# Optimization experiments

Hardware: AMD Instinct MI355X
Metric: run time of the kernel (lower is better)

Reference implementation:

```python
import jax, jax.numpy as jnp
import numpy as np
import math

EMBED_DIM = 1024
NUM_HEADS = 16
HEAD_DIM = EMBED_DIM // NUM_HEADS
B, S = 2, 2048


def setup_inputs() -> dict:
    key = jax.random.key(0)
    ks = jax.random.split(key, 5)
    scale = 1.0 / math.sqrt(EMBED_DIM)
    x = jax.random.normal(ks[0], (B, S, EMBED_DIM), dtype=jnp.float32)
    W_q = jax.random.normal(ks[1], (EMBED_DIM, EMBED_DIM), dtype=jnp.float32) * scale
    W_k = jax.random.normal(ks[2], (EMBED_DIM, EMBED_DIM), dtype=jnp.float32) * scale
    W_v = jax.random.normal(ks[3], (EMBED_DIM, EMBED_DIM), dtype=jnp.float32) * scale
    W_o = jax.random.normal(ks[4], (EMBED_DIM, EMBED_DIM), dtype=jnp.float32) * scale
    # causal mask: True = masked out (matches torch masked_fill semantics)
    mask = jnp.triu(jnp.ones((S, S), dtype=bool), k=1)
    return {"x": x, "mask": mask, "W_q": W_q, "W_k": W_k, "W_v": W_v, "W_o": W_o}


def _split_heads(x):
    b, s, _ = x.shape
    return x.reshape(b, s, NUM_HEADS, HEAD_DIM).transpose(0, 2, 1, 3)  # [b,h,s,hd]


def reference(x, mask, W_q, W_k, W_v, W_o):
    # torch nn.Linear(bias=False): y = x @ W.T
    Q = _split_heads(x @ W_q.T)
    K = _split_heads(x @ W_k.T)
    V = _split_heads(x @ W_v.T)
    scale = 1.0 / math.sqrt(HEAD_DIM)
    scores = jnp.einsum("bhqd,bhkd->bhqk", Q, K) * scale  # [b,h,s,s]
    scores = jnp.where(mask[None, None, :, :], -jnp.inf, scores)
    weights = jax.nn.softmax(scores, axis=-1)
    out = jnp.einsum("bhqk,bhkd->bhqd", weights, V)
    out = out.transpose(0, 2, 1, 3).reshape(x.shape[0], x.shape[1], EMBED_DIM)
    return out @ W_o.T
```

## Files before the change

kernel.cpp:

```cpp
#include <hip/hip_runtime.h>
#include <hip/hip_bf16.h>

typedef short bf16x8 __attribute__((ext_vector_type(8)));
typedef unsigned short u16x8 __attribute__((ext_vector_type(8)));
typedef unsigned short u16x4 __attribute__((ext_vector_type(4)));
typedef float f32x4 __attribute__((ext_vector_type(4)));

typedef unsigned int __attribute__((address_space(1))) gu32;
typedef unsigned int __attribute__((address_space(3))) lu32;

#define MFMA16(a, b, c) __builtin_amdgcn_mfma_f32_16x16x32_bf16((a), (b), (c), 0, 0, 0)

constexpr int SEQ = 2048;
constexpr int NH = 16;
constexpr int NTOK = 2 * SEQ;

__device__ __forceinline__ float bf2f(unsigned short u) {
  union { unsigned int i; float f; } v; v.i = ((unsigned int)u) << 16; return v.f;
}
__device__ __forceinline__ unsigned short f2bf(float f) {
  __hip_bfloat16 h = __float2bfloat16(f);
  return __builtin_bit_cast(unsigned short, h);
}
__device__ __forceinline__ unsigned int pkbf_trunc(float hi, float lo) {
  return __builtin_amdgcn_perm(__builtin_bit_cast(unsigned int, hi),
                               __builtin_bit_cast(unsigned int, lo), 0x07060302u);
}
__device__ __forceinline__ u16x8 cvt8(const float* __restrict__ p) {
  f32x4 a = *(const f32x4*)p;
  f32x4 b = *(const f32x4*)(p + 4);
  u16x8 r;
#pragma unroll
  for (int j = 0; j < 4; j++) { r[j] = f2bf(a[j]); r[4 + j] = f2bf(b[j]); }
  return r;
}

__global__ __launch_bounds__(256) void cvt_all(
    const float* __restrict__ x, const float* __restrict__ wq, const float* __restrict__ wk,
    const float* __restrict__ wv, const float* __restrict__ wo,
    unsigned short* __restrict__ Xb, unsigned short* __restrict__ Wb) {
  const int z = blockIdx.y;
  const float* src = (z == 0) ? x : (z == 1) ? wq : (z == 2) ? wk : (z == 3) ? wv : wo;
  unsigned short* dst = (z == 0) ? Xb : Wb + (size_t)(z - 1) * 1024 * 1024;
  const int n = (z == 0) ? NTOK * 1024 : 1024 * 1024;
  for (int i = (blockIdx.x * 256 + threadIdx.x) * 8; i < n; i += gridDim.x * 256 * 8)
    *(u16x8*)(dst + i) = cvt8(src + i);
}

template <int ROWS, int NWAVE>
__device__ __forceinline__ void stage_glds(const unsigned short* __restrict__ gbase,
                                           int rstride,
                                           unsigned short* __restrict__ lds,
                                           int wid, int lane) {
  constexpr int ISS = ROWS * 8 / (NWAVE * 64);
#pragma unroll
  for (int t = 0; t < ISS; ++t) {
    const int slot = (wid * ISS + t) * 64 + lane;
    const int row = slot >> 3;
    const int c8 = (slot & 7) ^ (row & 7);
    const unsigned short* gp = gbase + (size_t)row * rstride + c8 * 8;
    unsigned short* lp = lds + (size_t)(wid * ISS + t) * 512;
    __builtin_amdgcn_global_load_lds((const gu32*)gp, (lu32*)lp, 16, 0, 0);
  }
}

__device__ __forceinline__ bf16x8 frag_ld(const unsigned short* __restrict__ lds, int row, int c8) {
  const int slot = row * 8 + (c8 ^ (row & 7));
  return *(const bf16x8*)(lds + slot * 8);
}

template <int BM, int BN, int LDC, bool CF32>
__global__ __launch_bounds__(256) void gemm_lds(
    const unsigned short* __restrict__ A,
    const unsigned short* __restrict__ B,
    void* __restrict__ Cv) {
  constexpr int K = 1024;
  constexpr int MI = BM / 32, NI = BN / 32;

  __shared__ __align__(16) unsigned short As[BM * 64];
  __shared__ __align__(16) unsigned short Bs[BN * 64];

  const int tid = threadIdx.x;
  const int wid = tid >> 6;
  const int lane = tid & 63;
  const int quad = lane >> 4;
  const int c16 = lane & 15;
  const int wrow = wid >> 1, wcol = wid & 1;

  const int m0 = blockIdx.x * BM;
  const int n0 = blockIdx.y * BN;

  f32x4 acc[MI][NI];
#pragma unroll
  for (int i = 0; i < MI; i++)
#pragma unroll
    for (int j = 0; j < NI; j++) acc[i][j] = f32x4{0.f, 0.f, 0.f, 0.f};

  for (int kb = 0; kb < K; kb += 64) {
    __syncthreads();
    stage_glds<BM, 4>(A + (size_t)m0 * K + kb, K, As, wid, lane);
    stage_glds<BN, 4>(B + (size_t)n0 * K + kb, K, Bs, wid, lane);
    __syncthreads();
#pragma unroll
    for (int ks = 0; ks < 2; ++ks) {
      bf16x8 af[MI], bfr[NI];
#pragma unroll
      for (int i = 0; i < MI; i++)
        af[i] = frag_ld(As, wrow * (BM / 2) + i * 16 + c16, ks * 4 + quad);
#pragma unroll
      for (int j = 0; j < NI; j++)
        bfr[j] = frag_ld(Bs, wcol * (BN / 2) + j * 16 + c16, ks * 4 + quad);
#pragma unroll
      for (int i = 0; i < MI; i++)
#pragma unroll
        for (int j = 0; j < NI; j++) acc[i][j] = MFMA16(af[i], bfr[j], acc[i][j]);
    }
  }

#pragma unroll
  for (int i = 0; i < MI; i++) {
#pragma unroll
    for (int j = 0; j < NI; j++) {
      int row = m0 + wrow * (BM / 2) + i * 16 + quad * 4;
      int col = n0 + wcol * (BN / 2) + j * 16 + c16;
#pragma unroll
      for (int r = 0; r < 4; r++) {
        if constexpr (CF32) ((float*)Cv)[(size_t)(row + r) * LDC + col] = acc[i][j][r];
        else ((unsigned short*)Cv)[(size_t)(row + r) * LDC + col] = f2bf(acc[i][j][r]);
      }
    }
  }
}

__device__ __forceinline__ int vt_idx(int d, int kv) {
  int ck = kv >> 3;
  int s = ((d >> 3) ^ d) & 7;
  return d * 64 + ((ck ^ s) << 3) + (kv & 7);
}

struct AttnShared {
  unsigned short Kt[2][64 * 64];
  unsigned short Vt[64 * 64];
  unsigned short Pt[4][16 * 72];
};

__global__ __launch_bounds__(256) void attn_kernel(
    const unsigned short* __restrict__ QKV,
    unsigned short* __restrict__ Oa) {
  __shared__ AttnShared sh;
  const int h = blockIdx.x;
  const int b = blockIdx.y;
  const int t = 31 - blockIdx.z;
  const int tid = threadIdx.x;
  const int wid = tid >> 6, lane = tid & 63;
  const int quad = lane >> 4, c16 = lane & 15;
  const size_t tokbase = (size_t)b * SEQ;
  const int q0 = t * 64;
  const int nkv = t + 1;

  const unsigned short* qp = QKV + (tokbase + q0 + wid * 16 + c16) * 3072 + h * 64;
  bf16x8 qf[2];
#pragma unroll
  for (int ks = 0; ks < 2; ++ks) {
    u16x8 u = *(const u16x8*)(qp + ks * 32 + quad * 8);
    bf16x8 tq;
#pragma unroll
    for (int j = 0; j < 8; j++) tq[j] = (short)f2bf(0.1803368801f * bf2f(u[j]));
    qf[ks] = tq;
  }

  const unsigned short* kbase = QKV + tokbase * 3072 + 1024 + h * 64;
  const unsigned short* vbase = QKV + tokbase * 3072 + 2048 + h * 64;
  const int vkv = (tid >> 4) * 4;
  const int vd = (tid & 15) * 4;

  f32x4 o[4];
  float lacc = 0.f;
#pragma unroll
  for (int nt = 0; nt < 4; nt++) o[nt] = f32x4{0.f, 0.f, 0.f, 0.f};
  unsigned short* PtW = sh.Pt[wid];

  stage_glds<64, 4>(kbase, 3072, sh.Kt[0], wid, lane);
  u16x4 vr[4];
#pragma unroll
  for (int i = 0; i < 4; i++)
    vr[i] = *(const u16x4*)(vbase + (size_t)(vkv + i) * 3072 + vd);

  for (int kt = 0; kt < nkv; ++kt) {
    const int buf = kt & 1;
    __syncthreads();
#pragma unroll
    for (int dd = 0; dd < 4; ++dd) {
      uint2 w;
      w.x = (unsigned int)vr[0][dd] | ((unsigned int)vr[1][dd] << 16);
      w.y = (unsigned int)vr[2][dd] | ((unsigned int)vr[3][dd] << 16);
      *(uint2*)&sh.Vt[vt_idx(vd + dd, vkv)] = w;
    }
    __syncthreads();

    if (kt + 1 < nkv) {
      const size_t nofs = (size_t)(kt + 1) * 64;
      stage_glds<64, 4>(kbase + nofs * 3072, 3072, sh.Kt[buf ^ 1], wid, lane);
#pragma unroll
      for (int i = 0; i < 4; i++)
        vr[i] = *(const u16x4*)(vbase + (nofs + vkv + i) * 3072 + vd);
    }

    const unsigned short* KtB = sh.Kt[buf];
    f32x4 st[4];
#pragma unroll
    for (int nt = 0; nt < 4; ++nt) {
      f32x4 a = f32x4{-16.f, -16.f, -16.f, -16.f};
      a = MFMA16(frag_ld(KtB, nt * 16 + c16, quad), qf[0], a);
      a = MFMA16(frag_ld(KtB, nt * 16 + c16, 4 + quad), qf[1], a);
      st[nt] = a;
    }
    if (kt == nkv - 1) {
      const int kv0 = kt * 64;
      const int qg = q0 + wid * 16 + c16;
#pragma unroll
      for (int nt = 0; nt < 4; nt++)
#pragma unroll
        for (int r = 0; r < 4; r++) {
          int kg = kv0 + nt * 16 + quad * 4 + r;
          if (kg > qg) st[nt][r] = -1e30f;
        }
    }

#pragma unroll
    for (int nt = 0; nt < 4; nt++) {
      float p0 = __builtin_amdgcn_exp2f(st[nt][0]);
      float p1 = __builtin_amdgcn_exp2f(st[nt][1]);
      float p2 = __builtin_amdgcn_exp2f(st[nt][2]);
      float p3 = __builtin_amdgcn_exp2f(st[nt][3]);
      lacc += (p0 + p1) + (p2 + p3);
      uint2 w;
      w.x = pkbf_trunc(p1, p0);
      w.y = pkbf_trunc(p3, p2);
      *(uint2*)&PtW[c16 * 72 + nt * 16 + quad * 4] = w;
    }

#pragma unroll
    for (int ks = 0; ks < 2; ++ks) {
      bf16x8 pf = *(const bf16x8*)&PtW[c16 * 72 + ks * 32 + quad * 8];
#pragma unroll
      for (int nt2 = 0; nt2 < 4; ++nt2) {
        bf16x8 vf = *(const bf16x8*)&sh.Vt[vt_idx(nt2 * 16 + c16, ks * 32 + quad * 8)];
        o[nt2] = MFMA16(vf, pf, o[nt2]);
      }
    }
  }

  lacc += __shfl_xor(lacc, 16);
  lacc += __shfl_xor(lacc, 32);
  const float linv = 1.f / lacc;
  const size_t row = tokbase + q0 + wid * 16 + c16;
#pragma unroll
  for (int nt2 = 0; nt2 < 4; nt2++) {
    uint2 w;
    w.x = (unsigned int)f2bf(o[nt2][0] * linv) | ((unsigned int)f2bf(o[nt2][1] * linv) << 16);
    w.y = (unsigned int)f2bf(o[nt2][2] * linv) | ((unsigned int)f2bf(o[nt2][3] * linv) << 16);
    *(uint2*)&Oa[row * 1024 + h * 64 + nt2 * 16 + quad * 4] = w;
  }
}

template <int BM, int BN, int LDC, bool AF32, bool CF32>
__global__ __launch_bounds__(256) void gemm_bt(
    const void* __restrict__ Av, const float* __restrict__ W0, const float* __restrict__ W1,
    const float* __restrict__ W2, void* __restrict__ Cv) {
  constexpr int K = 1024;
  constexpr int LDS_LD = 72;
  constexpr int MI = BM / 32, NI = BN / 32;
  __shared__ __align__(16) unsigned short As[BM][LDS_LD];
  __shared__ __align__(16) unsigned short Bs[BN][LDS_LD];
  const int tid = threadIdx.x, wid = tid >> 6, lane = tid & 63;
  const int quad = lane >> 4, c16 = lane & 15;
  const int wrow = wid >> 1, wcol = wid & 1;
  const float* W = (blockIdx.z == 0) ? W0 : (blockIdx.z == 1 ? W1 : W2);
  const int m0 = blockIdx.y * BM, n0 = blockIdx.x * BN, cofs = blockIdx.z * 1024;
  f32x4 acc[MI][NI];
#pragma unroll
  for (int i = 0; i < MI; i++)
#pragma unroll
    for (int j = 0; j < NI; j++) acc[i][j] = f32x4{0.f, 0.f, 0.f, 0.f};
  for (int kb = 0; kb < K; kb += 64) {
    __syncthreads();
#pragma unroll
    for (int c = tid; c < BM * 8; c += 256) {
      int row = c >> 3, c8 = c & 7;
      if constexpr (AF32)
        *(u16x8*)&As[row][c8 * 8] = cvt8((const float*)Av + (size_t)(m0 + row) * K + kb + c8 * 8);
      else
        *(u16x8*)&As[row][c8 * 8] = *(const u16x8*)((const unsigned short*)Av + (size_t)(m0 + row) * K + kb + c8 * 8);
    }
#pragma unroll
    for (int c = tid; c < BN * 8; c += 256) {
      int row = c >> 3, c8 = c & 7;
      *(u16x8*)&Bs[row][c8 * 8] = cvt8(W + (size_t)(n0 + row) * K + kb + c8 * 8);
    }
    __syncthreads();
#pragma unroll
    for (int ks = 0; ks < 2; ++ks) {
      bf16x8 af[MI], bfr[NI];
#pragma unroll
      for (int i = 0; i < MI; i++)
        af[i] = *(const bf16x8*)&As[wrow * (BM / 2) + i * 16 + c16][ks * 32 + quad * 8];
#pragma unroll
      for (int j = 0; j < NI; j++)
        bfr[j] = *(const bf16x8*)&Bs[wcol * (BN / 2) + j * 16 + c16][ks * 32 + quad * 8];
#pragma unroll
      for (int i = 0; i < MI; i++)
#pragma unroll
        for (int j = 0; j < NI; j++) acc[i][j] = MFMA16(af[i], bfr[j], acc[i][j]);
    }
  }
#pragma unroll
  for (int i = 0; i < MI; i++)
#pragma unroll
    for (int j = 0; j < NI; j++) {
      int row = m0 + wrow * (BM / 2) + i * 16 + quad * 4;
      int col = n0 + wcol * (BN / 2) + j * 16 + c16 + cofs;
#pragma unroll
      for (int r = 0; r < 4; r++) {
        if constexpr (CF32) ((float*)Cv)[(size_t)(row + r) * LDC + col] = acc[i][j][r];
        else ((unsigned short*)Cv)[(size_t)(row + r) * LDC + col] = f2bf(acc[i][j][r]);
      }
    }
}

extern "C" void kernel_launch(void* const* d_in, const int* in_sizes, int n_in,
                              void* d_out, int out_size, void* d_ws, size_t ws_size,
                              hipStream_t stream) {
  const float* x = (const float*)d_in[0];
  const float* Wq = (const float*)d_in[2];
  const float* Wk = (const float*)d_in[3];
  const float* Wv = (const float*)d_in[4];
  const float* Wo = (const float*)d_in[5];
  float* out = (float*)d_out;

  unsigned short* QKV = (unsigned short*)d_ws;
  unsigned short* Wb = QKV + (size_t)NTOK * 3072;
  unsigned short* Xb = Wb + (size_t)4 * 1024 * 1024;
  unsigned short* AT = Xb;

  if (ws_size >= (size_t)40 * 1024 * 1024) {
    cvt_all<<<dim3(256, 5), 256, 0, stream>>>(x, Wq, Wk, Wv, Wo, Xb, Wb);
    gemm_lds<128, 64, 3072, false><<<dim3(32, 48), 256, 0, stream>>>(Xb, Wb, QKV);
    attn_kernel<<<dim3(NH, 2, 32), 256, 0, stream>>>(QKV, AT);
    gemm_lds<128, 64, 1024, true><<<dim3(32, 16), 256, 0, stream>>>(
        AT, Wb + (size_t)3 * 1024 * 1024, out);
  } else {
    unsigned short* QKV2 = (unsigned short*)d_ws;
    unsigned short* AT2 = QKV2 + (size_t)NTOK * 3072;
    gemm_bt<128, 128, 3072, true, false><<<dim3(8, 32, 3), 256, 0, stream>>>(x, Wq, Wk, Wv, QKV2);
    attn_kernel<<<dim3(NH, 2, 32), 256, 0, stream>>>(QKV2, AT2);
    gemm_bt<64, 64, 1024, false, true><<<dim3(16, 64, 1), 256, 0, stream>>>(AT2, Wo, Wo, Wo, out);
  }
}
```

Measured before the change: 182.8 us.

## Replace QKV projection GEMM with 256x256-tile eight-phase pipelined kernel

Adds a new QKV projection GEMM that uses 256x256 output tiles with 512 threads and double-buffered LDS filled by direct global-to-LDS loads. The loop is split into eight phases, interleaving fragment loads, async stage issues, and prioritized MFMA blocks between explicit barriers, with an XCD-aware block swizzle over 192 blocks. The aim is higher data reuse per tile and overlap of memory traffic with matrix math in the largest GEMM. The cost is 128 KB of LDS per block, many barriers, and only 192 blocks, which is below one wave of blocks per CU.

```diff
diff --git a/kernel.cpp b/kernel.cpp
--- a/kernel.cpp
+++ b/kernel.cpp
@@ -128,6 +128,140 @@
         if constexpr (CF32) ((float*)Cv)[(size_t)(row + r) * LDC + col] = acc[i][j][r];
         else ((unsigned short*)Cv)[(size_t)(row + r) * LDC + col] = f2bf(acc[i][j][r]);
       }
+    }
+  }
+}
+
+#define SBAR do { __builtin_amdgcn_sched_barrier(0); \
+                  asm volatile("s_barrier" ::: "memory"); \
+                  __builtin_amdgcn_sched_barrier(0); } while (0)
+
+__global__ __launch_bounds__(512) void gemm_8ph(
+    const unsigned short* __restrict__ A,
+    const unsigned short* __restrict__ B,
+    unsigned short* __restrict__ C) {
+  constexpr int K = 1024;
+  __shared__ __align__(16) unsigned short As[2][256 * 64];
+  __shared__ __align__(16) unsigned short Bs[2][256 * 64];
+
+  const int tid = threadIdx.x;
+  const int wid = tid >> 6, lane = tid & 63;
+  const int quad = lane >> 4, c16 = lane & 15;
+  const int wr = wid >> 2;
+  const int wc = wid & 3;
+
+  const int bid = blockIdx.x;
+  const int swz = (bid & 7) * 24 + (bid >> 3);
+  const int m0 = (swz / 12) * 256;
+  const int n0 = (swz % 12) * 256;
+
+  const unsigned short* Abase = A + (size_t)m0 * K;
+  const unsigned short* Bbase = B + (size_t)n0 * K;
+
+  f32x4 acc[8][4];
+#pragma unroll
+  for (int i = 0; i < 8; i++)
+#pragma unroll
+    for (int j = 0; j < 4; j++) acc[i][j] = f32x4{0.f, 0.f, 0.f, 0.f};
+
+  bf16x8 af[4][2];
+  bf16x8 bf0[2][2];
+  bf16x8 bf1[2][2];
+
+  auto lda = [&](const unsigned short* asb, int mo) {
+#pragma unroll
+    for (int mi = 0; mi < 4; mi++)
+#pragma unroll
+      for (int ks = 0; ks < 2; ks++)
+        af[mi][ks] = frag_ld(asb, wr * 128 + mo + mi * 16 + c16, ks * 4 + quad);
+  };
+  auto ldb = [&](const unsigned short* bsb, bf16x8 (&bf)[2][2], int no) {
+#pragma unroll
+    for (int ni = 0; ni < 2; ni++)
+#pragma unroll
+      for (int ks = 0; ks < 2; ks++)
+        bf[ni][ks] = frag_ld(bsb, wc * 64 + no + ni * 16 + c16, ks * 4 + quad);
+  };
+  auto mmq = [&](bf16x8 (&bf)[2][2], int mo, int no) {
+    __builtin_amdgcn_s_setprio(1);
+#pragma unroll
+    for (int mi = 0; mi < 4; mi++)
+#pragma unroll
+      for (int ni = 0; ni < 2; ni++)
+#pragma unroll
+        for (int ks = 0; ks < 2; ks++)
+          acc[mo + mi][no + ni] = MFMA16(af[mi][ks], bf[ni][ks], acc[mo + mi][no + ni]);
+    __builtin_amdgcn_s_setprio(0);
+  };
+
+  stage_glds<128, 8>(Bbase, K, Bs[0], wid, lane);
+  stage_glds<128, 8>(Bbase + (size_t)128 * K, K, Bs[0] + 8192, wid, lane);
+  stage_glds<128, 8>(Abase, K, As[0], wid, lane);
+  stage_glds<128, 8>(Abase + (size_t)128 * K, K, As[0] + 8192, wid, lane);
+  stage_glds<128, 8>(Bbase + 64, K, Bs[1], wid, lane);
+  stage_glds<128, 8>(Bbase + (size_t)128 * K + 64, K, Bs[1] + 8192, wid, lane);
+  asm volatile("s_waitcnt vmcnt(4)" ::: "memory");
+  SBAR;
+
+  for (int i = 0; i < 7; ++i) {
+    const int t = 2 * i;
+    const int kb1 = (t + 1) * 64, kb2 = (t + 2) * 64, kb3 = (t + 3) * 64;
+    lda(As[0], 0); ldb(Bs[0], bf0, 0);
+    stage_glds<128, 8>(Abase + kb1, K, As[1], wid, lane);
+    SBAR; mmq(bf0, 0, 0); SBAR;
+    ldb(Bs[0], bf1, 32);
+    stage_glds<128, 8>(Abase + (size_t)128 * K + kb1, K, As[1] + 8192, wid, lane);
+    SBAR; mmq(bf1, 0, 2); SBAR;
+    lda(As[0], 64);
+    stage_glds<128, 8>(Bbase + kb2, K, Bs[0], wid, lane);
+    SBAR; mmq(bf0, 4, 0); SBAR;
+    stage_glds<128, 8>(Bbase + (size_t)128 * K + kb2, K, Bs[0] + 8192, wid, lane);
+    asm volatile("s_waitcnt vmcnt(4)" ::: "memory");
+    SBAR; mmq(bf1, 4, 2); SBAR;
+    lda(As[1], 0); ldb(Bs[1], bf0, 0);
+    stage_glds<128, 8>(Abase + kb2, K, As[0], wid, lane);
+    SBAR; mmq(bf0, 0, 0); SBAR;
+    ldb(Bs[1], bf1, 32);
+    stage_glds<128, 8>(Abase + (size_t)128 * K + kb2, K, As[0] + 8192, wid, lane);
+    SBAR; mmq(bf1, 0, 2); SBAR;
+    lda(As[1], 64);
+    stage_glds<128, 8>(Bbase + kb3, K, Bs[1], wid, lane);
+    SBAR; mmq(bf0, 4, 0); SBAR;
+    stage_glds<128, 8>(Bbase + (size_t)128 * K + kb3, K, Bs[1] + 8192, wid, lane);
+    asm volatile("s_waitcnt vmcnt(4)" ::: "memory");
+    SBAR; mmq(bf1, 4, 2); SBAR;
+  }
+
+  {
+    const int kb1 = 15 * 64;
+    lda(As[0], 0); ldb(Bs[0], bf0, 0);
+    stage_glds<128, 8>(Abase + kb1, K, As[1], wid, lane);
+    SBAR; mmq(bf0, 0, 0); SBAR;
+    ldb(Bs[0], bf1, 32);
+    stage_glds<128, 8>(Abase + (size_t)128 * K + kb1, K, As[1] + 8192, wid, lane);
+    SBAR; mmq(bf1, 0, 2); SBAR;
+    lda(As[0], 64);
+    SBAR; mmq(bf0, 4, 0); SBAR;
+    asm volatile("s_waitcnt vmcnt(0)" ::: "memory");
+    SBAR; mmq(bf1, 4, 2); SBAR;
+    lda(As[1], 0); ldb(Bs[1], bf0, 0);
+    SBAR; mmq(bf0, 0, 0); SBAR;
+    ldb(Bs[1], bf1, 32);
+    SBAR; mmq(bf1, 0, 2); SBAR;
+    lda(As[1], 64);
+    SBAR; mmq(bf0, 4, 0); SBAR;
+    SBAR; mmq(bf1, 4, 2);
+  }
+
+#pragma unroll
+  for (int mi = 0; mi < 8; mi++) {
+#pragma unroll
+    for (int ni = 0; ni < 4; ni++) {
+      const int row = m0 + wr * 128 + mi * 16 + quad * 4;
+      const int col = n0 + wc * 64 + ni * 16 + c16;
+#pragma unroll
+      for (int r = 0; r < 4; r++)
+        C[(size_t)(row + r) * 3072 + col] = f2bf(acc[mi][ni][r]);
     }
   }
 }
@@ -345,7 +479,7 @@
 
   if (ws_size >= (size_t)40 * 1024 * 1024) {
     cvt_all<<<dim3(256, 5), 256, 0, stream>>>(x, Wq, Wk, Wv, Wo, Xb, Wb);
-    gemm_lds<128, 64, 3072, false><<<dim3(32, 48), 256, 0, stream>>>(Xb, Wb, QKV);
+    gemm_8ph<<<dim3(192), 512, 0, stream>>>(Xb, Wb, QKV);
     attn_kernel<<<dim3(NH, 2, 32), 256, 0, stream>>>(QKV, AT);
     gemm_lds<128, 64, 1024, true><<<dim3(32, 16), 256, 0, stream>>>(
         AT, Wb + (size_t)3 * 1024 * 1024, out);
```

Result: faster. 178.8 us (-2.2%).

## Replace QKV projection GEMM with 256x192 eight-phase pipelined kernel

Applied to the files above, without the earlier changes.

Adds a new 512-thread QKV GEMM with 256x192 output tiles, double-buffered LDS, async global-to-LDS staging interleaved with MFMA phases under explicit barriers and vmcnt waits, and a swizzled block order. It targets the latency and low reuse of the previous 128x64 tile GEMM. It also raises wave priority around the MFMA sections in the attention kernel. The hand-scheduled phases depend on exact vmcnt accounting and use a large LDS footprint, which limits occupancy.

```diff
diff --git a/kernel.cpp b/kernel.cpp
--- a/kernel.cpp
+++ b/kernel.cpp
@@ -128,6 +128,134 @@
         if constexpr (CF32) ((float*)Cv)[(size_t)(row + r) * LDC + col] = acc[i][j][r];
         else ((unsigned short*)Cv)[(size_t)(row + r) * LDC + col] = f2bf(acc[i][j][r]);
       }
+    }
+  }
+}
+
+#define SBAR do { __builtin_amdgcn_sched_barrier(0); \
+                  asm volatile("s_barrier" ::: "memory"); \
+                  __builtin_amdgcn_sched_barrier(0); } while (0)
+
+__global__ __launch_bounds__(512) void gemm_8ph_w192(
+    const unsigned short* __restrict__ A,
+    const unsigned short* __restrict__ B,
+    unsigned short* __restrict__ C) {
+  constexpr int K = 1024;
+  __shared__ __align__(16) unsigned short As[2][256 * 64];
+  __shared__ __align__(16) unsigned short Bs[2][192 * 64];
+
+  const int tid = threadIdx.x;
+  const int wid = tid >> 6, lane = tid & 63;
+  const int quad = lane >> 4, c16 = lane & 15;
+  const int wr = wid >> 2;
+  const int wc = wid & 3;
+
+  const int bid = blockIdx.x;
+  const int swz = (bid & 7) * 32 + (bid >> 3);
+  const int m0 = (swz >> 4) * 256;
+  const int n0 = (swz & 15) * 192;
+
+  const unsigned short* Abase = A + (size_t)m0 * K;
+  const unsigned short* Bbase = B + (size_t)n0 * K;
+
+  f32x4 acc[8][3];
+#pragma unroll
+  for (int i = 0; i < 8; i++)
+#pragma unroll
+    for (int j = 0; j < 3; j++) acc[i][j] = f32x4{0.f, 0.f, 0.f, 0.f};
+
+  bf16x8 af[4];
+  bf16x8 bf0[3];
+  bf16x8 bf1[3];
+
+  auto lda4 = [&](const unsigned short* asb, int mo, int ks) {
+#pragma unroll
+    for (int mi = 0; mi < 4; mi++)
+      af[mi] = frag_ld(asb, wr * 128 + (mo + mi) * 16 + c16, ks * 4 + quad);
+  };
+  auto ldb3 = [&](const unsigned short* bsb, bf16x8 (&bf)[3], int ks) {
+#pragma unroll
+    for (int ni = 0; ni < 3; ni++)
+      bf[ni] = frag_ld(bsb, wc * 48 + ni * 16 + c16, ks * 4 + quad);
+  };
+  auto mm12 = [&](bf16x8 (&bf)[3], int mo) {
+    __builtin_amdgcn_s_setprio(1);
+#pragma unroll
+    for (int mi = 0; mi < 4; mi++)
+#pragma unroll
+      for (int ni = 0; ni < 3; ni++)
+        acc[mo + mi][ni] = MFMA16(af[mi], bf[ni], acc[mo + mi][ni]);
+    __builtin_amdgcn_s_setprio(0);
+  };
+
+  stage_glds<192, 8>(Bbase, K, Bs[0], wid, lane);
+  stage_glds<128, 8>(Abase, K, As[0], wid, lane);
+  stage_glds<128, 8>(Abase + (size_t)128 * K, K, As[0] + 8192, wid, lane);
+  stage_glds<192, 8>(Bbase + 64, K, Bs[1], wid, lane);
+  asm volatile("s_waitcnt vmcnt(3)" ::: "memory");
+  SBAR;
+
+  for (int i = 0; i < 7; ++i) {
+    const int t = 2 * i;
+    const int kb1 = (t + 1) * 64, kb2 = (t + 2) * 64, kb3 = (t + 3) * 64;
+    lda4(As[0], 0, 0); ldb3(Bs[0], bf0, 0);
+    stage_glds<128, 8>(Abase + kb1, K, As[1], wid, lane);
+    SBAR; mm12(bf0, 0); SBAR;
+    lda4(As[0], 0, 1); ldb3(Bs[0], bf1, 1);
+    stage_glds<128, 8>(Abase + (size_t)128 * K + kb1, K, As[1] + 8192, wid, lane);
+    SBAR; mm12(bf1, 0); SBAR;
+    lda4(As[0], 4, 0);
+    stage_glds<192, 8>(Bbase + kb2, K, Bs[0], wid, lane);
+    SBAR; mm12(bf0, 4); SBAR;
+    lda4(As[0], 4, 1);
+    asm volatile("s_waitcnt vmcnt(3)" ::: "memory");
+    SBAR; mm12(bf1, 4); SBAR;
+    lda4(As[1], 0, 0); ldb3(Bs[1], bf0, 0);
+    stage_glds<128, 8>(Abase + kb2, K, As[0], wid, lane);
+    SBAR; mm12(bf0, 0); SBAR;
+    lda4(As[1], 0, 1); ldb3(Bs[1], bf1, 1);
+    stage_glds<128, 8>(Abase + (size_t)128 * K + kb2, K, As[0] + 8192, wid, lane);
+    SBAR; mm12(bf1, 0); SBAR;
+    lda4(As[1], 4, 0);
+    stage_glds<192, 8>(Bbase + kb3, K, Bs[1], wid, lane);
+    SBAR; mm12(bf0, 4); SBAR;
+    lda4(As[1], 4, 1);
+    asm volatile("s_waitcnt vmcnt(3)" ::: "memory");
+    SBAR; mm12(bf1, 4); SBAR;
+  }
+
+  {
+    const int kb1 = 15 * 64;
+    lda4(As[0], 0, 0); ldb3(Bs[0], bf0, 0);
+    stage_glds<128, 8>(Abase + kb1, K, As[1], wid, lane);
+    SBAR; mm12(bf0, 0); SBAR;
+    lda4(As[0], 0, 1); ldb3(Bs[0], bf1, 1);
+    stage_glds<128, 8>(Abase + (size_t)128 * K + kb1, K, As[1] + 8192, wid, lane);
+    SBAR; mm12(bf1, 0); SBAR;
+    lda4(As[0], 4, 0);
+    SBAR; mm12(bf0, 4); SBAR;
+    lda4(As[0], 4, 1);
+    asm volatile("s_waitcnt vmcnt(0)" ::: "memory");
+    SBAR; mm12(bf1, 4); SBAR;
+    lda4(As[1], 0, 0); ldb3(Bs[1], bf0, 0);
+    SBAR; mm12(bf0, 0); SBAR;
+    lda4(As[1], 0, 1); ldb3(Bs[1], bf1, 1);
+    SBAR; mm12(bf1, 0); SBAR;
+    lda4(As[1], 4, 0);
+    SBAR; mm12(bf0, 4); SBAR;
+    lda4(As[1], 4, 1);
+    SBAR; mm12(bf1, 4);
+  }
+
+#pragma unroll
+  for (int mi = 0; mi < 8; mi++) {
+#pragma unroll
+    for (int ni = 0; ni < 3; ni++) {
+      const int row = m0 + wr * 128 + mi * 16 + quad * 4;
+      const int col = n0 + wc * 48 + ni * 16 + c16;
+#pragma unroll
+      for (int r = 0; r < 4; r++)
+        C[(size_t)(row + r) * 3072 + col] = f2bf(acc[mi][ni][r]);
     }
   }
 }
@@ -208,6 +336,7 @@
 
     const unsigned short* KtB = sh.Kt[buf];
     f32x4 st[4];
+    __builtin_amdgcn_s_setprio(1);
 #pragma unroll
     for (int nt = 0; nt < 4; ++nt) {
       f32x4 a = f32x4{-16.f, -16.f, -16.f, -16.f};
@@ -215,6 +344,7 @@
       a = MFMA16(frag_ld(KtB, nt * 16 + c16, 4 + quad), qf[1], a);
       st[nt] = a;
     }
+    __builtin_amdgcn_s_setprio(0);
     if (kt == nkv - 1) {
       const int kv0 = kt * 64;
       const int qg = q0 + wid * 16 + c16;
@@ -240,6 +370,7 @@
       *(uint2*)&PtW[c16 * 72 + nt * 16 + quad * 4] = w;
     }
 
+    __builtin_amdgcn_s_setprio(1);
 #pragma unroll
     for (int ks = 0; ks < 2; ++ks) {
       bf16x8 pf = *(const bf16x8*)&PtW[c16 * 72 + ks * 32 + quad * 8];
@@ -249,6 +380,7 @@
         o[nt2] = MFMA16(vf, pf, o[nt2]);
       }
     }
+    __builtin_amdgcn_s_setprio(0);
   }
 
   lacc += __shfl_xor(lacc, 16);
@@ -345,7 +477,7 @@
 
   if (ws_size >= (size_t)40 * 1024 * 1024) {
     cvt_all<<<dim3(256, 5), 256, 0, stream>>>(x, Wq, Wk, Wv, Wo, Xb, Wb);
-    gemm_lds<128, 64, 3072, false><<<dim3(32, 48), 256, 0, stream>>>(Xb, Wb, QKV);
+    gemm_8ph_w192<<<dim3(256), 512, 0, stream>>>(Xb, Wb, QKV);
     attn_kernel<<<dim3(NH, 2, 32), 256, 0, stream>>>(QKV, AT);
     gemm_lds<128, 64, 1024, true><<<dim3(32, 16), 256, 0, stream>>>(
         AT, Wb + (size_t)3 * 1024 * 1024, out);
```

New measurement: 175.2 us. -4.2%, faster.
